# Performance work log

Hardware: AMD Instinct MI355X
Metric: run time of the kernel (lower is better)

The kernel has to match this reference:

```python
import jax, jax.numpy as jnp
import numpy as np

B, S, W = 64, 128, 16
VOCAB, CVOCAB = 50000, 100
WDIM, CDIM, NF = 300, 50, 50
KS = [3, 4, 5]
HID, NLAYERS, NLAB = 256, 2, 5
COMB = WDIM + NF * len(KS)  # 450


def glorot(key, shape):
    fan_in, fan_out = shape[-2], shape[-1]
    lim = jnp.sqrt(6.0 / (fan_in + fan_out))
    return jax.random.uniform(key, shape, minval=-lim, maxval=lim, dtype=jnp.float32)


def setup_inputs() -> dict:
    key = jax.random.key(0)
    ks = jax.random.split(key, 32)
    word_ids = jax.random.randint(ks[0], (B, S), 1, VOCAB)
    char_ids = jax.random.randint(ks[1], (B, S, W), 1, CVOCAB)
    labels = jax.random.randint(ks[2], (B, S), 0, NLAB)
    lengths = jax.random.randint(ks[3], (B,), S // 2, S + 1)
    # embeddings
    word_emb = jax.random.normal(ks[4], (VOCAB, WDIM), jnp.float32) * 0.1
    word_emb = word_emb.at[0].set(0.0)
    char_emb = jax.random.normal(ks[5], (CVOCAB, CDIM), jnp.float32) * 0.1
    char_emb = char_emb.at[0].set(0.0)
    # char conv kernels: [ks, CDIM, NF] each, plus bias
    conv_w = [glorot(ks[6 + i], (k, CDIM, NF)) for i, k in enumerate(KS)]
    conv_b = [jnp.zeros((NF,), jnp.float32) for _ in KS]
    # LSTM params per layer per direction: W_ih [in,4H], W_hh [H,4H], b [4H]
    lstm = []
    kidx = 10
    in_dim = COMB
    for layer in range(NLAYERS):
        for d in range(2):
            Wih = glorot(ks[kidx], (in_dim, 4 * HID)); kidx += 1
            Whh = glorot(ks[kidx], (HID, 4 * HID)); kidx += 1
            b = jnp.zeros((4 * HID,), jnp.float32)
            lstm.extend([Wih, Whh, b])
        in_dim = 2 * HID
    out_w = glorot(ks[kidx], (2 * HID, NLAB)); kidx += 1
    out_b = jnp.zeros((NLAB,), jnp.float32)
    crf_start = jax.random.normal(ks[kidx], (NLAB,), jnp.float32) * 0.1; kidx += 1
    crf_end = jax.random.normal(ks[kidx], (NLAB,), jnp.float32) * 0.1; kidx += 1
    crf_trans = jax.random.normal(ks[kidx], (NLAB, NLAB), jnp.float32) * 0.1
    d = {
        'word_ids': word_ids, 'char_ids': char_ids, 'labels': labels, 'lengths': lengths,
        'word_emb': word_emb, 'char_emb': char_emb,
        'conv_w3': conv_w[0], 'conv_b3': conv_b[0],
        'conv_w4': conv_w[1], 'conv_b4': conv_b[1],
        'conv_w5': conv_w[2], 'conv_b5': conv_b[2],
        'out_w': out_w, 'out_b': out_b,
        'crf_start': crf_start, 'crf_end': crf_end, 'crf_trans': crf_trans,
    }
    names = ['Wih', 'Whh', 'b']
    i = 0
    for layer in range(NLAYERS):
        for dname in ['f', 'r']:
            for n in names:
                d[f'lstm_{n}_l{layer}{dname}'] = lstm[i]; i += 1
    return d


def _conv1d_same(x, w, b, pad):
    # x: [N, L, Cin], w: [k, Cin, Cout] -> [N, L_out, Cout]
    out = jax.lax.conv_general_dilated(x, w, window_strides=(1,), padding=[(pad, pad)],
                                       dimension_numbers=('NWC', 'WIO', 'NWC'))
    return out + b


def _lstm_dir(x, Wih, Whh, b, reverse):
    # x: [B, S, in] -> [B, S, H]; gate order i,f,g,o (torch convention)
    xg = jnp.einsum('bsi,ij->bsj', x, Wih) + b  # [B,S,4H]
    if reverse:
        xg = xg[:, ::-1]
    def step(carry, g):
        h, c = carry
        g = g + h @ Whh
        i, f, gg, o = jnp.split(g, 4, axis=-1)
        i, f, o = jax.nn.sigmoid(i), jax.nn.sigmoid(f), jax.nn.sigmoid(o)
        c = f * c + i * jnp.tanh(gg)
        h = o * jnp.tanh(c)
        return (h, c), h
    h0 = jnp.zeros((x.shape[0], HID), x.dtype)
    _, hs = jax.lax.scan(step, (h0, h0), jnp.swapaxes(xg, 0, 1))
    hs = jnp.swapaxes(hs, 0, 1)
    if reverse:
        hs = hs[:, ::-1]
    return hs


def reference(word_ids, char_ids, labels, lengths, word_emb, char_emb,
              conv_w3, conv_b3, conv_w4, conv_b4, conv_w5, conv_b5,
              out_w, out_b, crf_start, crf_end, crf_trans,
              lstm_Wih_l0f, lstm_Whh_l0f, lstm_b_l0f,
              lstm_Wih_l0r, lstm_Whh_l0r, lstm_b_l0r,
              lstm_Wih_l1f, lstm_Whh_l1f, lstm_b_l1f,
              lstm_Wih_l1r, lstm_Whh_l1r, lstm_b_l1r):
    # char CNN
    ce = char_emb[char_ids.reshape(-1, W)]  # [B*S, W, CDIM]
    pooled = []
    for w, b, k in [(conv_w3, conv_b3, 3), (conv_w4, conv_b4, 4), (conv_w5, conv_b5, 5)]:
        o = jax.nn.relu(_conv1d_same(ce, w, b, k // 2))
        pooled.append(jnp.max(o, axis=1))  # [B*S, NF]
    char_repr = jnp.concatenate(pooled, axis=-1).reshape(B, S, NF * len(KS))
    we = word_emb[word_ids]
    x = jnp.concatenate([we, char_repr], axis=-1)  # [B,S,COMB]
    # BiLSTM 2 layers (dropout disabled / eval mode)
    h_f = _lstm_dir(x, lstm_Wih_l0f, lstm_Whh_l0f, lstm_b_l0f, False)
    h_r = _lstm_dir(x, lstm_Wih_l0r, lstm_Whh_l0r, lstm_b_l0r, True)
    x = jnp.concatenate([h_f, h_r], axis=-1)
    h_f = _lstm_dir(x, lstm_Wih_l1f, lstm_Whh_l1f, lstm_b_l1f, False)
    h_r = _lstm_dir(x, lstm_Wih_l1r, lstm_Whh_l1r, lstm_b_l1r, True)
    x = jnp.concatenate([h_f, h_r], axis=-1)
    emissions = jnp.einsum('bsh,hl->bsl', x, out_w) + out_b  # [B,S,NLAB]
    # CRF NLL (pytorch-crf, batch_first, reduction='mean')
    mask = (jnp.arange(S)[None, :] < lengths[:, None])  # [B,S] bool
    maskf = mask.astype(emissions.dtype)
    tags = labels  # already in [0,NLAB)
    # numerator: score of gold path
    em_score = jnp.take_along_axis(emissions, tags[..., None], axis=-1)[..., 0]  # [B,S]
    num = crf_start[tags[:, 0]] + em_score[:, 0]
    trans_score = crf_trans[tags[:, :-1], tags[:, 1:]]  # [B,S-1]
    num = num + jnp.sum((trans_score + em_score[:, 1:]) * maskf[:, 1:], axis=1)
    last_idx = lengths - 1
    last_tag = jnp.take_along_axis(tags, last_idx[:, None], axis=1)[:, 0]
    num = num + crf_end[last_tag]
    # denominator: forward algorithm via scan
    alpha0 = crf_start + emissions[:, 0]  # [B,NLAB]
    def step(alpha, inp):
        em_t, m_t = inp  # [B,NLAB], [B]
        nxt = jax.nn.logsumexp(alpha[:, :, None] + crf_trans[None], axis=1) + em_t
        alpha = jnp.where(m_t[:, None], nxt, alpha)
        return alpha, None
    alpha, _ = jax.lax.scan(step, alpha0,
                            (jnp.swapaxes(emissions[:, 1:], 0, 1), jnp.swapaxes(mask[:, 1:], 0, 1)))
    denom = jax.nn.logsumexp(alpha + crf_end[None], axis=1)  # [B]
    llh = num - denom
    return -jnp.mean(llh)
```

## Files before the change

### kernel.cpp

```cpp
#include <hip/hip_runtime.h>
#include <hip/hip_fp16.h>
#include <math.h>
#include <stdint.h>

#define NB   64
#define NS   128
#define NW   16
#define CD   50
#define NF_  50
#define WD   300
#define COMB 450
#define K2P0 240
#define K2P1 256
#define HID  256
#define G4   1024
#define NLAB 5

#define WHH_SW4  (7.0f / 0.06846532f)
#define WHH_INV4 (1.0f / (WHH_SW4 * 7.0f))

typedef _Float16 h2_t __attribute__((ext_vector_type(2)));
typedef _Float16 v8h  __attribute__((ext_vector_type(8)));
typedef float    v16f __attribute__((ext_vector_type(16)));

__device__ __forceinline__ float sigf(float x)   { return 1.0f / (1.0f + __expf(-x)); }
__device__ __forceinline__ float tanhf_(float x) { return 1.0f - 2.0f / (__expf(2.0f * x) + 1.0f); }

__device__ __forceinline__ float dot2f(uint32_t a, uint32_t b, float c) {
#if __has_builtin(__builtin_amdgcn_fdot2)
    return __builtin_amdgcn_fdot2(__builtin_bit_cast(h2_t, a),
                                  __builtin_bit_cast(h2_t, b), c, false);
#else
    h2_t ah = __builtin_bit_cast(h2_t, a), bh = __builtin_bit_cast(h2_t, b);
    return c + (float)ah[0] * (float)bh[0] + (float)ah[1] * (float)bh[1];
#endif
}

__device__ __forceinline__ int sdot8f(uint32_t a, int b, int acc) {
#if __has_builtin(__builtin_amdgcn_sdot8)
    return __builtin_amdgcn_sdot8((int)a, b, acc, false);
#else
#pragma unroll
    for (int i = 0; i < 8; ++i) {
        int av = ((int)(a << (28 - 4 * i))) >> 28;
        int bv = ((int)(((uint32_t)b) << (28 - 4 * i))) >> 28;
        acc += av * bv;
    }
    return acc;
#endif
}

__device__ __forceinline__ uint32_t packh2(float lo, float hi) {
    __half l = __float2half(lo), h = __float2half(hi);
    return ((uint32_t)__half_as_ushort(h) << 16) | (uint32_t)__half_as_ushort(l);
}

__global__ __launch_bounds__(256) void pack_convw(
    const float* __restrict__ w3, const float* __restrict__ w4,
    const float* __restrict__ w5, uint32_t* __restrict__ cwp)
{
    int idx = blockIdx.x * 256 + threadIdx.x;
    if (idx >= 15000) return;
    const float* W; int rel;
    if (idx < 3750)       { W = w3; rel = idx; }
    else if (idx < 8750)  { W = w4; rel = idx - 3750; }
    else                  { W = w5; rel = idx - 8750; }
    int t = rel / 1250, rem = rel - t * 1250;
    int c2 = rem / 50, f = rem - c2 * 50;
    float lo = W[(size_t)t * (CD * NF_) + (2 * c2) * NF_ + f];
    float hi = W[(size_t)t * (CD * NF_) + (2 * c2 + 1) * NF_ + f];
    cwp[idx] = packh2(lo, hi);
}

__global__ __launch_bounds__(512) void cnn_embed3(
    const int* __restrict__ word_ids, const int* __restrict__ char_ids,
    const float* __restrict__ word_emb, const float* __restrict__ char_emb,
    const uint32_t* __restrict__ cwp,
    const float* __restrict__ b3, const float* __restrict__ b4,
    const float* __restrict__ b5, uint32_t* __restrict__ x0p)
{
    __shared__ uint32_t cws[15000];
    __shared__ uint32_t cep[8][NW][25];
    int tid  = threadIdx.x;
    int g    = tid >> 6;
    int lane = tid & 63;
    int pos  = blockIdx.x * 8 + g;

    for (int i = tid; i < 15000; i += 512) cws[i] = cwp[i];

    const int* cid = char_ids + (size_t)pos * NW;
    for (int idx = lane; idx < NW * 25; idx += 64) {
        int w  = idx / 25;
        int c2 = idx - w * 25;
        const float* e = char_emb + (size_t)cid[w] * CD + 2 * c2;
        cep[g][w][c2] = packh2(e[0], e[1]);
    }
    {
        int wid = word_ids[pos];
        const float* src = word_emb + (size_t)wid * WD;
        uint32_t* dst = x0p + (size_t)pos * K2P0;
        for (int idx = lane; idx < 150; idx += 64) {
            float2 v = *(const float2*)(src + 2 * idx);
            dst[idx] = packh2(v.x, v.y);
        }
        for (int idx = lane; idx < 15; idx += 64) dst[225 + idx] = 0;
    }
    __syncthreads();

    int f = lane;
    float m3 = 0.f, m4 = 0.f, m5 = 0.f;
    if (f < NF_) {
        float a3[16], a4[17], a5[16];
        float bb3 = b3[f], bb4 = b4[f], bb5 = b5[f];
#pragma unroll
        for (int p = 0; p < 16; ++p) { a3[p] = bb3; a5[p] = bb5; }
#pragma unroll
        for (int p = 0; p < 17; ++p) a4[p] = bb4;

        for (int c2 = 0; c2 < 25; ++c2) {
            uint32_t w3r[3], w4r[4], w5r[5];
#pragma unroll
            for (int t = 0; t < 3; ++t) w3r[t] = cws[(t * 25 + c2) * NF_ + f];
#pragma unroll
            for (int t = 0; t < 4; ++t) w4r[t] = cws[3750 + (t * 25 + c2) * NF_ + f];
#pragma unroll
            for (int t = 0; t < 5; ++t) w5r[t] = cws[8750 + (t * 25 + c2) * NF_ + f];
#pragma unroll
            for (int ip = 0; ip < 16; ++ip) {
                uint32_t v = cep[g][ip][c2];
#pragma unroll
                for (int t = 0; t < 3; ++t) { int p = ip + 1 - t; if (p >= 0 && p < 16) a3[p] = dot2f(v, w3r[t], a3[p]); }
#pragma unroll
                for (int t = 0; t < 4; ++t) { int p = ip + 2 - t; if (p >= 0 && p < 17) a4[p] = dot2f(v, w4r[t], a4[p]); }
#pragma unroll
                for (int t = 0; t < 5; ++t) { int p = ip + 2 - t; if (p >= 0 && p < 16) a5[p] = dot2f(v, w5r[t], a5[p]); }
            }
        }
#pragma unroll
        for (int p = 0; p < 16; ++p) m3 = fmaxf(m3, a3[p]);
#pragma unroll
        for (int p = 0; p < 17; ++p) m4 = fmaxf(m4, a4[p]);
#pragma unroll
        for (int p = 0; p < 16; ++p) m5 = fmaxf(m5, a5[p]);
    }
    float m3x = __shfl_xor(m3, 1);
    float m4x = __shfl_xor(m4, 1);
    float m5x = __shfl_xor(m5, 1);
    if (f < NF_ && !(f & 1)) {
        int i = f >> 1;
        uint32_t* dst = x0p + (size_t)pos * K2P0 + 150;
        dst[i]      = packh2(m3, m3x);
        dst[25 + i] = packh2(m4, m4x);
        dst[50 + i] = packh2(m5, m5x);
    }
}

__global__ __launch_bounds__(256) void pack_wih_all(
    const float* __restrict__ W0f, const float* __restrict__ W0r,
    const float* __restrict__ W1f, const float* __restrict__ W1r,
    uint32_t* __restrict__ P0f, uint32_t* __restrict__ P0r,
    uint32_t* __restrict__ P1f, uint32_t* __restrict__ P1r)
{
    int layer = blockIdx.z;
    int K   = layer ? 512 : COMB;
    int K2P = layer ? K2P1 : K2P0;
    const float* W = layer ? (blockIdx.y ? W1r : W1f) : (blockIdx.y ? W0r : W0f);
    uint32_t* P    = layer ? (blockIdx.y ? P1r : P1f) : (blockIdx.y ? P0r : P0f);

    int idx = blockIdx.x * 256 + threadIdx.x;
    if (idx >= K2P * 1024) return;
    int n = idx & 1023, kp = idx >> 10;
    uint32_t v = 0;
    if (2 * kp + 1 < K) {
        __half l = __float2half(W[(size_t)(2 * kp) * 1024 + n]);
        __half h = __float2half(W[(size_t)(2 * kp + 1) * 1024 + n]);
        v = ((uint32_t)__half_as_ushort(h) << 16) | (uint32_t)__half_as_ushort(l);
    }
    P[((size_t)(kp >> 2) * 1024 + n) * 4 + (kp & 3)] = v;
}

__global__ __launch_bounds__(256) void pack_whh_i4(
    const float* __restrict__ W0, const float* __restrict__ W1,
    const float* __restrict__ W2, const float* __restrict__ W3,
    uint32_t* __restrict__ Q0, uint32_t* __restrict__ Q1,
    uint32_t* __restrict__ Q2, uint32_t* __restrict__ Q3)
{
    int idx = blockIdx.x * 256 + threadIdx.x;
    if (idx >= 32768) return;
    const float* W; uint32_t* Q;
    switch (blockIdx.y) {
        case 0:  W = W0; Q = Q0; break;
        case 1:  W = W1; Q = Q1; break;
        case 2:  W = W2; Q = Q2; break;
        default: W = W3; Q = Q3; break;
    }
    int m = idx & 3, col = (idx >> 2) & 1023, iq = idx >> 12;
    int kbase = (iq * 4 + m) * 8;
    uint32_t out = 0;
#pragma unroll
    for (int j = 0; j < 8; ++j) {
        float w = W[(size_t)(kbase + j) * G4 + col];
        int q = (int)rintf(w * WHH_SW4);
        q = q < -7 ? -7 : (q > 7 ? 7 : q);
        out |= ((uint32_t)(q & 0xF)) << (4 * j);
    }
    Q[idx] = out;
}

__global__ __launch_bounds__(256) void gemm_mfma(
    const uint32_t* __restrict__ Ap, int K2,
    const uint32_t* __restrict__ Wpf, const uint32_t* __restrict__ Wpr,
    const float* __restrict__ bf, const float* __restrict__ br,
    float* __restrict__ Cf, float* __restrict__ Cr)
{
    int by  = blockIdx.y;
    int dir = by >> 4;
    int n0  = (by & 15) * 64;
    int m0  = blockIdx.x * 128;
    const uint32_t* Wp = dir ? Wpr : Wpf;
    const float* bias  = dir ? br : bf;
    float* C           = dir ? Cr : Cf;

    int tid = threadIdx.x;
    int w = tid >> 6, l = tid & 63;
    int l31 = l & 31, lk = l >> 5;

    const uint32_t* arow = Ap + (size_t)(m0 + w * 32 + l31) * K2 + lk * 4;
    const uint4*    bq0  = (const uint4*)(Wp) + (size_t)lk * 1024 + n0 + l31;

    v16f acc0 = {}, acc1 = {};

    for (int kp0 = 0; kp0 < K2; kp0 += 8) {
        uint4 av = *(const uint4*)(arow + kp0);
        const uint4* bq = bq0 + (size_t)(kp0 >> 2) * 1024;
        uint4 b0v = bq[0];
        uint4 b1v = bq[32];
        v8h af = __builtin_bit_cast(v8h, av);
        acc0 = __builtin_amdgcn_mfma_f32_32x32x16_f16(af, __builtin_bit_cast(v8h, b0v), acc0, 0, 0, 0);
        acc1 = __builtin_amdgcn_mfma_f32_32x32x16_f16(af, __builtin_bit_cast(v8h, b1v), acc1, 0, 0, 0);
    }

#pragma unroll
    for (int r = 0; r < 16; ++r) {
        int row = m0 + w * 32 + (r & 3) + 8 * (r >> 2) + 4 * lk;
        int c0 = n0 + l31, c1 = n0 + 32 + l31;
        C[(size_t)row * G4 + c0] = acc0[r] + bias[c0];
        C[(size_t)row * G4 + c1] = acc1[r] + bias[c1];
    }
}

__global__ __launch_bounds__(512, 1) void lstm_rec12(
    const float* __restrict__ xg_f, const float* __restrict__ xg_r,
    const uint32_t* __restrict__ Qf, const uint32_t* __restrict__ Qr,
    uint32_t* __restrict__ outp)
{
    int bid = blockIdx.x;
    int b = bid >> 1, d = bid & 1;
    const float* xg = d ? xg_r : xg_f;
    const uint4* Q4 = (const uint4*)(d ? Qr : Qf);

    __shared__ uint32_t hp8[32];
    __shared__ float gates[G4];
    __shared__ alignas(16) uint4 Tl[4 * 1024];

    int t = threadIdx.x;
    int lane = t & 63;

    uint4 rA[4], rB[4];
#pragma unroll
    for (int iq = 0; iq < 4; ++iq) {
        rA[iq] = Q4[(size_t)iq * 1024 + t];
        rB[iq] = Q4[(size_t)iq * 1024 + t + 512];
    }
    for (int i = t; i < 4 * 1024; i += 512) Tl[i] = Q4[4 * 1024 + i];
    if (t < 32) hp8[t] = 0;
    float cst = 0.f;
    __syncthreads();

    for (int s = 0; s < NS; ++s) {
        int te = d ? (NS - 1 - s) : s;
        int row = b * NS + te;
        size_t r0 = (size_t)row * G4;
        float xA = xg[r0 + t];
        float xB = xg[r0 + 512 + t];

        int hreg = (int)hp8[lane & 31];
        int a0 = 0, a1 = 0;

#pragma unroll
        for (int iq = 0; iq < 4; ++iq) {
            int h0 = __builtin_amdgcn_readlane(hreg, 4 * iq);
            int h1 = __builtin_amdgcn_readlane(hreg, 4 * iq + 1);
            int h2 = __builtin_amdgcn_readlane(hreg, 4 * iq + 2);
            int h3 = __builtin_amdgcn_readlane(hreg, 4 * iq + 3);
            a0 = sdot8f(rA[iq].x, h0, a0); a0 = sdot8f(rA[iq].y, h1, a0);
            a0 = sdot8f(rA[iq].z, h2, a0); a0 = sdot8f(rA[iq].w, h3, a0);
            a1 = sdot8f(rB[iq].x, h0, a1); a1 = sdot8f(rB[iq].y, h1, a1);
            a1 = sdot8f(rB[iq].z, h2, a1); a1 = sdot8f(rB[iq].w, h3, a1);
        }
#pragma unroll
        for (int iq2 = 0; iq2 < 4; ++iq2) {
            uint4 wa = Tl[iq2 * 1024 + t];
            uint4 wb = Tl[iq2 * 1024 + t + 512];
            int h0 = __builtin_amdgcn_readlane(hreg, 16 + 4 * iq2);
            int h1 = __builtin_amdgcn_readlane(hreg, 17 + 4 * iq2);
            int h2 = __builtin_amdgcn_readlane(hreg, 18 + 4 * iq2);
            int h3 = __builtin_amdgcn_readlane(hreg, 19 + 4 * iq2);
            a0 = sdot8f(wa.x, h0, a0); a0 = sdot8f(wa.y, h1, a0);
            a0 = sdot8f(wa.z, h2, a0); a0 = sdot8f(wa.w, h3, a0);
            a1 = sdot8f(wb.x, h0, a1); a1 = sdot8f(wb.y, h1, a1);
            a1 = sdot8f(wb.z, h2, a1); a1 = sdot8f(wb.w, h3, a1);
        }

        gates[t]       = (float)a0 * WHH_INV4 + xA;
        gates[t + 512] = (float)a1 * WHH_INV4 + xB;
        __syncthreads();
        if (t < 256) {
            int j = t;
            float gi = gates[j];
            float gf = gates[256 + j];
            float gg = gates[512 + j];
            float go = gates[768 + j];
            float ii = sigf(gi), ff = sigf(gf), g2 = tanhf_(gg), oo = sigf(go);
            cst = ff * cst + ii * g2;
            float h = oo * tanhf_(cst);
            int q = (int)rintf(h * 7.0f);
            q = q < -7 ? -7 : (q > 7 ? 7 : q);
            int qx = __shfl_xor(q, 1);
            float hx = __shfl_xor(h, 1);
            if (!(t & 1)) {
                ((unsigned char*)hp8)[j >> 1] =
                    (unsigned char)((q & 0xF) | ((qx & 0xF) << 4));
                outp[(size_t)row * 256 + d * 128 + (j >> 1)] = packh2(h, hx);
            }
        }
        __syncthreads();
    }
}

__global__ __launch_bounds__(256) void emis_kernel(
    const uint32_t* __restrict__ x2p, const float* __restrict__ ow,
    const float* __restrict__ ob, float* __restrict__ em)
{
    int i = blockIdx.x * blockDim.x + threadIdx.x;
    if (i >= NB * NS) return;
    const uint32_t* xr = x2p + (size_t)i * 256;
    float acc[NLAB];
#pragma unroll
    for (int l = 0; l < NLAB; ++l) acc[l] = ob[l];
    for (int p = 0; p < 256; ++p) {
        h2_t hv = __builtin_bit_cast(h2_t, xr[p]);
        float lo = (float)hv[0], hi = (float)hv[1];
        int k = 2 * p;
#pragma unroll
        for (int l = 0; l < NLAB; ++l)
            acc[l] += lo * ow[(size_t)k * NLAB + l] + hi * ow[(size_t)(k + 1) * NLAB + l];
    }
    float* e = em + (size_t)i * NLAB;
#pragma unroll
    for (int l = 0; l < NLAB; ++l) e[l] = acc[l];
}

__device__ __forceinline__ float lse5(const float* v) {
    float m = fmaxf(fmaxf(fmaxf(v[0], v[1]), fmaxf(v[2], v[3])), v[4]);
    float s = __expf(v[0] - m) + __expf(v[1] - m) + __expf(v[2] - m) +
              __expf(v[3] - m) + __expf(v[4] - m);
    return m + __logf(s);
}

__global__ __launch_bounds__(64) void crf_kernel(
    const float* __restrict__ em, const int* __restrict__ labels,
    const int* __restrict__ lengths, const float* __restrict__ cstart,
    const float* __restrict__ cend, const float* __restrict__ ctrans,
    float* __restrict__ outp)
{
    __shared__ float tr_s[25], st_s[5], en_s[5];
    int tid = threadIdx.x;
    if (tid < 25) tr_s[tid] = ctrans[tid];
    if (tid < 5)  { st_s[tid] = cstart[tid]; en_s[tid] = cend[tid]; }
    __syncthreads();

    int b = tid;
    int len = lengths[b];
    const int* tg = labels + (size_t)b * NS;
    const float* eb = em + (size_t)b * NS * NLAB;

    int prev = tg[0];
    float num = st_s[prev] + eb[prev];
    for (int t = 1; t < NS; ++t) {
        if (t < len) {
            int cur = tg[t];
            num += tr_s[prev * NLAB + cur] + eb[t * NLAB + cur];
            prev = cur;
        }
    }
    num += en_s[tg[len - 1]];

    float a[NLAB];
#pragma unroll
    for (int y = 0; y < NLAB; ++y) a[y] = st_s[y] + eb[y];
    for (int t = 1; t < NS; ++t) {
        if (t < len) {
            float na[NLAB];
#pragma unroll
            for (int y = 0; y < NLAB; ++y) {
                float v[NLAB];
#pragma unroll
                for (int x = 0; x < NLAB; ++x) v[x] = a[x] + tr_s[x * NLAB + y];
                na[y] = lse5(v) + eb[t * NLAB + y];
            }
#pragma unroll
            for (int y = 0; y < NLAB; ++y) a[y] = na[y];
        }
    }
    float v[NLAB];
#pragma unroll
    for (int y = 0; y < NLAB; ++y) v[y] = a[y] + en_s[y];
    float denom = lse5(v);

    float llh = num - denom;
#pragma unroll
    for (int off = 32; off > 0; off >>= 1) llh += __shfl_down(llh, off);
    if (tid == 0) outp[0] = -llh * (1.0f / 64.0f);
}

extern "C" void kernel_launch(void* const* d_in, const int* in_sizes, int n_in,
                              void* d_out, int out_size, void* d_ws, size_t ws_size,
                              hipStream_t stream)
{
    const int*   word_ids = (const int*)d_in[0];
    const int*   char_ids = (const int*)d_in[1];
    const int*   labels   = (const int*)d_in[2];
    const int*   lengths  = (const int*)d_in[3];
    const float* word_emb = (const float*)d_in[4];
    const float* char_emb = (const float*)d_in[5];
    const float* cw3 = (const float*)d_in[6];
    const float* cb3 = (const float*)d_in[7];
    const float* cw4 = (const float*)d_in[8];
    const float* cb4 = (const float*)d_in[9];
    const float* cw5 = (const float*)d_in[10];
    const float* cb5 = (const float*)d_in[11];
    const float* out_w = (const float*)d_in[12];
    const float* out_b = (const float*)d_in[13];
    const float* crf_start = (const float*)d_in[14];
    const float* crf_end   = (const float*)d_in[15];
    const float* crf_trans = (const float*)d_in[16];
    const float* Wih_l0f = (const float*)d_in[17];
    const float* Whh_l0f = (const float*)d_in[18];
    const float* b_l0f   = (const float*)d_in[19];
    const float* Wih_l0r = (const float*)d_in[20];
    const float* Whh_l0r = (const float*)d_in[21];
    const float* b_l0r   = (const float*)d_in[22];
    const float* Wih_l1f = (const float*)d_in[23];
    const float* Whh_l1f = (const float*)d_in[24];
    const float* b_l1f   = (const float*)d_in[25];
    const float* Wih_l1r = (const float*)d_in[26];
    const float* Whh_l1r = (const float*)d_in[27];
    const float* b_l1r   = (const float*)d_in[28];

    uint32_t* wsu = (uint32_t*)d_ws;
    uint32_t* x0p  = wsu;
    float*    xg_f = (float*)(wsu + 1966080);
    float*    xg_r = xg_f + 8388608;
    uint32_t* x1p  = (uint32_t*)(xg_r + 8388608);
    uint32_t* x2p  = x1p + 2097152;
    float*    em   = (float*)(x2p + 2097152);
    uint32_t* wp0f = (uint32_t*)(em + 40960);
    uint32_t* wp0r = wp0f + 245760;
    uint32_t* wp1f = wp0r + 245760;
    uint32_t* wp1r = wp1f + 262144;
    uint32_t* cwp  = wp1r + 262144;
    uint32_t* wh0f = x0p;
    uint32_t* wh0r = wh0f + 32768;
    uint32_t* wh1f = wh0r + 32768;
    uint32_t* wh1r = wh1f + 32768;

    pack_convw<<<59, 256, 0, stream>>>(cw3, cw4, cw5, cwp);

    cnn_embed3<<<1024, 512, 0, stream>>>(word_ids, char_ids, word_emb, char_emb,
                                         cwp, cb3, cb4, cb5, x0p);

    pack_wih_all<<<dim3(1024, 2, 2), 256, 0, stream>>>(
        Wih_l0f, Wih_l0r, Wih_l1f, Wih_l1r, wp0f, wp0r, wp1f, wp1r);

    dim3 gGemm(64, 32);
    gemm_mfma<<<gGemm, 256, 0, stream>>>(x0p, K2P0, wp0f, wp0r, b_l0f, b_l0r, xg_f, xg_r);

    pack_whh_i4<<<dim3(128, 4), 256, 0, stream>>>(Whh_l0f, Whh_l0r, Whh_l1f, Whh_l1r,
                                                  wh0f, wh0r, wh1f, wh1r);

    lstm_rec12<<<128, 512, 0, stream>>>(xg_f, xg_r, wh0f, wh0r, x1p);

    gemm_mfma<<<gGemm, 256, 0, stream>>>(x1p, K2P1, wp1f, wp1r, b_l1f, b_l1r, xg_f, xg_r);

    lstm_rec12<<<128, 512, 0, stream>>>(xg_f, xg_r, wh1f, wh1r, x2p);

    emis_kernel<<<32, 256, 0, stream>>>(x2p, out_w, out_b, em);
    crf_kernel<<<1, 64, 0, stream>>>(em, labels, lengths, crf_start, crf_end, crf_trans,
                                     (float*)d_out);
}
```

Baseline: 545.7 us.

## Interleave LSTM gate columns so each step needs one barrier, merge pack kernels

The recurrent Whh packing permutes gate columns so that adjacent lanes hold matching i/f/g/o gate values for the same hidden unit. Gate activations are then combined through shuffles instead of a shared-memory gates array, and the hidden state is double-buffered. This removes one __syncthreads and the LDS round trip per timestep. It also splits the sdot8 accumulators to shorten the dependency chain, and fuses the three weight-pack kernels into one launch, moving the Whh packed buffer so it no longer aliases x0p.

Measured after the change: 550.2 us. No clear change (+0.8%).

```diff
diff --git a/kernel.cpp b/kernel.cpp
--- a/kernel.cpp
+++ b/kernel.cpp
@@ -55,21 +55,81 @@
     return ((uint32_t)__half_as_ushort(h) << 16) | (uint32_t)__half_as_ushort(l);
 }
 
-__global__ __launch_bounds__(256) void pack_convw(
+#define PK_CONV_END 59
+#define PK_WIH0_END (59 + 1920)
+#define PK_WIH1_END (PK_WIH0_END + 2048)
+#define PK_END      (PK_WIH1_END + 512)
+
+__global__ __launch_bounds__(256) void pack_all(
     const float* __restrict__ w3, const float* __restrict__ w4,
-    const float* __restrict__ w5, uint32_t* __restrict__ cwp)
-{
-    int idx = blockIdx.x * 256 + threadIdx.x;
-    if (idx >= 15000) return;
-    const float* W; int rel;
-    if (idx < 3750)       { W = w3; rel = idx; }
-    else if (idx < 8750)  { W = w4; rel = idx - 3750; }
-    else                  { W = w5; rel = idx - 8750; }
-    int t = rel / 1250, rem = rel - t * 1250;
-    int c2 = rem / 50, f = rem - c2 * 50;
-    float lo = W[(size_t)t * (CD * NF_) + (2 * c2) * NF_ + f];
-    float hi = W[(size_t)t * (CD * NF_) + (2 * c2 + 1) * NF_ + f];
-    cwp[idx] = packh2(lo, hi);
+    const float* __restrict__ w5, uint32_t* __restrict__ cwp,
+    const float* __restrict__ Wih0f, const float* __restrict__ Wih0r,
+    const float* __restrict__ Wih1f, const float* __restrict__ Wih1r,
+    uint32_t* __restrict__ P0f, uint32_t* __restrict__ P0r,
+    uint32_t* __restrict__ P1f, uint32_t* __restrict__ P1r,
+    const float* __restrict__ Whh0f, const float* __restrict__ Whh0r,
+    const float* __restrict__ Whh1f, const float* __restrict__ Whh1r,
+    uint32_t* __restrict__ Q0f, uint32_t* __restrict__ Q0r,
+    uint32_t* __restrict__ Q1f, uint32_t* __restrict__ Q1r)
+{
+    int blk = blockIdx.x;
+    int tid = threadIdx.x;
+
+    if (blk < PK_CONV_END) {
+        int idx = blk * 256 + tid;
+        if (idx >= 15000) return;
+        const float* W; int rel;
+        if (idx < 3750)       { W = w3; rel = idx; }
+        else if (idx < 8750)  { W = w4; rel = idx - 3750; }
+        else                  { W = w5; rel = idx - 8750; }
+        int t = rel / 1250, rem = rel - t * 1250;
+        int c2 = rem / 50, f = rem - c2 * 50;
+        float lo = W[(size_t)t * (CD * NF_) + (2 * c2) * NF_ + f];
+        float hi = W[(size_t)t * (CD * NF_) + (2 * c2 + 1) * NF_ + f];
+        cwp[idx] = packh2(lo, hi);
+    } else if (blk < PK_WIH1_END) {
+        int layer, dir, rel;
+        if (blk < PK_WIH0_END) { layer = 0; rel = blk - PK_CONV_END; dir = rel / 960;  rel %= 960; }
+        else                   { layer = 1; rel = blk - PK_WIH0_END; dir = rel / 1024; rel %= 1024; }
+        int K   = layer ? 512 : COMB;
+        int K2P = layer ? K2P1 : K2P0;
+        const float* W = layer ? (dir ? Wih1r : Wih1f) : (dir ? Wih0r : Wih0f);
+        uint32_t* P    = layer ? (dir ? P1r : P1f) : (dir ? P0r : P0f);
+        int idx = rel * 256 + tid;
+        if (idx >= K2P * 1024) return;
+        int n = idx & 1023, kp = idx >> 10;
+        uint32_t v = 0;
+        if (2 * kp + 1 < K) {
+            __half l = __float2half(W[(size_t)(2 * kp) * 1024 + n]);
+            __half h = __float2half(W[(size_t)(2 * kp + 1) * 1024 + n]);
+            v = ((uint32_t)__half_as_ushort(h) << 16) | (uint32_t)__half_as_ushort(l);
+        }
+        P[((size_t)(kp >> 2) * 1024 + n) * 4 + (kp & 3)] = v;
+    } else {
+        int rel = blk - PK_WIH1_END;
+        int which = rel >> 7;
+        const float* W; uint32_t* Q;
+        switch (which) {
+            case 0:  W = Whh0f; Q = Q0f; break;
+            case 1:  W = Whh0r; Q = Q0r; break;
+            case 2:  W = Whh1f; Q = Q1f; break;
+            default: W = Whh1r; Q = Q1r; break;
+        }
+        int idx = (rel & 127) * 256 + tid;
+        int m = idx & 3, s = (idx >> 2) & 1023, iq = idx >> 12;
+        int sh = s & 511;
+        int L = ((s >> 9) << 9) + ((sh & 1) << 8) + (sh >> 1);
+        int kbase = (iq * 4 + m) * 8;
+        uint32_t out = 0;
+#pragma unroll
+        for (int j = 0; j < 8; ++j) {
+            float w = W[(size_t)(kbase + j) * G4 + L];
+            int q = (int)rintf(w * WHH_SW4);
+            q = q < -7 ? -7 : (q > 7 ? 7 : q);
+            out |= ((uint32_t)(q & 0xF)) << (4 * j);
+        }
+        Q[idx] = out;
+    }
 }
 
 __global__ __launch_bounds__(512) void cnn_embed3(
@@ -155,58 +215,6 @@
     }
 }
 
-__global__ __launch_bounds__(256) void pack_wih_all(
-    const float* __restrict__ W0f, const float* __restrict__ W0r,
-    const float* __restrict__ W1f, const float* __restrict__ W1r,
-    uint32_t* __restrict__ P0f, uint32_t* __restrict__ P0r,
-    uint32_t* __restrict__ P1f, uint32_t* __restrict__ P1r)
-{
-    int layer = blockIdx.z;
-    int K   = layer ? 512 : COMB;
-    int K2P = layer ? K2P1 : K2P0;
-    const float* W = layer ? (blockIdx.y ? W1r : W1f) : (blockIdx.y ? W0r : W0f);
-    uint32_t* P    = layer ? (blockIdx.y ? P1r : P1f) : (blockIdx.y ? P0r : P0f);
-
-    int idx = blockIdx.x * 256 + threadIdx.x;
-    if (idx >= K2P * 1024) return;
-    int n = idx & 1023, kp = idx >> 10;
-    uint32_t v = 0;
-    if (2 * kp + 1 < K) {
-        __half l = __float2half(W[(size_t)(2 * kp) * 1024 + n]);
-        __half h = __float2half(W[(size_t)(2 * kp + 1) * 1024 + n]);
-        v = ((uint32_t)__half_as_ushort(h) << 16) | (uint32_t)__half_as_ushort(l);
-    }
-    P[((size_t)(kp >> 2) * 1024 + n) * 4 + (kp & 3)] = v;
-}
-
-__global__ __launch_bounds__(256) void pack_whh_i4(
-    const float* __restrict__ W0, const float* __restrict__ W1,
-    const float* __restrict__ W2, const float* __restrict__ W3,
-    uint32_t* __restrict__ Q0, uint32_t* __restrict__ Q1,
-    uint32_t* __restrict__ Q2, uint32_t* __restrict__ Q3)
-{
-    int idx = blockIdx.x * 256 + threadIdx.x;
-    if (idx >= 32768) return;
-    const float* W; uint32_t* Q;
-    switch (blockIdx.y) {
-        case 0:  W = W0; Q = Q0; break;
-        case 1:  W = W1; Q = Q1; break;
-        case 2:  W = W2; Q = Q2; break;
-        default: W = W3; Q = Q3; break;
-    }
-    int m = idx & 3, col = (idx >> 2) & 1023, iq = idx >> 12;
-    int kbase = (iq * 4 + m) * 8;
-    uint32_t out = 0;
-#pragma unroll
-    for (int j = 0; j < 8; ++j) {
-        float w = W[(size_t)(kbase + j) * G4 + col];
-        int q = (int)rintf(w * WHH_SW4);
-        q = q < -7 ? -7 : (q > 7 ? 7 : q);
-        out |= ((uint32_t)(q & 0xF)) << (4 * j);
-    }
-    Q[idx] = out;
-}
-
 __global__ __launch_bounds__(256) void gemm_mfma(
     const uint32_t* __restrict__ Ap, int K2,
     const uint32_t* __restrict__ Wpf, const uint32_t* __restrict__ Wpr,
@@ -249,7 +257,7 @@
     }
 }
 
-__global__ __launch_bounds__(512, 1) void lstm_rec12(
+__global__ __launch_bounds__(512, 1) void lstm_rec13(
     const float* __restrict__ xg_f, const float* __restrict__ xg_r,
     const uint32_t* __restrict__ Qf, const uint32_t* __restrict__ Qr,
     uint32_t* __restrict__ outp)
@@ -259,12 +267,12 @@
     const float* xg = d ? xg_r : xg_f;
     const uint4* Q4 = (const uint4*)(d ? Qr : Qf);
 
-    __shared__ uint32_t hp8[32];
-    __shared__ float gates[G4];
+    __shared__ uint32_t hp8[2][32];
     __shared__ alignas(16) uint4 Tl[4 * 1024];
 
     int t = threadIdx.x;
     int lane = t & 63;
+    int Lt = ((t & 1) << 8) + (t >> 1);
 
     uint4 rA[4], rB[4];
 #pragma unroll
@@ -273,19 +281,20 @@
         rB[iq] = Q4[(size_t)iq * 1024 + t + 512];
     }
     for (int i = t; i < 4 * 1024; i += 512) Tl[i] = Q4[4 * 1024 + i];
-    if (t < 32) hp8[t] = 0;
-    float cst = 0.f;
+    if (t < 32) hp8[0][t] = 0;
+    float cst = 0.f, h = 0.f;
+    int q = 0;
     __syncthreads();
 
     for (int s = 0; s < NS; ++s) {
         int te = d ? (NS - 1 - s) : s;
         int row = b * NS + te;
         size_t r0 = (size_t)row * G4;
-        float xA = xg[r0 + t];
-        float xB = xg[r0 + 512 + t];
-
-        int hreg = (int)hp8[lane & 31];
-        int a0 = 0, a1 = 0;
+        float xA = xg[r0 + Lt];
+        float xB = xg[r0 + Lt + 512];
+
+        int hreg = (int)hp8[s & 1][lane & 31];
+        int a0a = 0, a0b = 0, a1a = 0, a1b = 0;
 
 #pragma unroll
         for (int iq = 0; iq < 4; ++iq) {
@@ -293,10 +302,10 @@
             int h1 = __builtin_amdgcn_readlane(hreg, 4 * iq + 1);
             int h2 = __builtin_amdgcn_readlane(hreg, 4 * iq + 2);
             int h3 = __builtin_amdgcn_readlane(hreg, 4 * iq + 3);
-            a0 = sdot8f(rA[iq].x, h0, a0); a0 = sdot8f(rA[iq].y, h1, a0);
-            a0 = sdot8f(rA[iq].z, h2, a0); a0 = sdot8f(rA[iq].w, h3, a0);
-            a1 = sdot8f(rB[iq].x, h0, a1); a1 = sdot8f(rB[iq].y, h1, a1);
-            a1 = sdot8f(rB[iq].z, h2, a1); a1 = sdot8f(rB[iq].w, h3, a1);
+            a0a = sdot8f(rA[iq].x, h0, a0a); a0b = sdot8f(rA[iq].y, h1, a0b);
+            a0a = sdot8f(rA[iq].z, h2, a0a); a0b = sdot8f(rA[iq].w, h3, a0b);
+            a1a = sdot8f(rB[iq].x, h0, a1a); a1b = sdot8f(rB[iq].y, h1, a1b);
+            a1a = sdot8f(rB[iq].z, h2, a1a); a1b = sdot8f(rB[iq].w, h3, a1b);
         }
 #pragma unroll
         for (int iq2 = 0; iq2 < 4; ++iq2) {
@@ -306,33 +315,30 @@
             int h1 = __builtin_amdgcn_readlane(hreg, 17 + 4 * iq2);
             int h2 = __builtin_amdgcn_readlane(hreg, 18 + 4 * iq2);
             int h3 = __builtin_amdgcn_readlane(hreg, 19 + 4 * iq2);
-            a0 = sdot8f(wa.x, h0, a0); a0 = sdot8f(wa.y, h1, a0);
-            a0 = sdot8f(wa.z, h2, a0); a0 = sdot8f(wa.w, h3, a0);
-            a1 = sdot8f(wb.x, h0, a1); a1 = sdot8f(wb.y, h1, a1);
-            a1 = sdot8f(wb.z, h2, a1); a1 = sdot8f(wb.w, h3, a1);
-        }
-
-        gates[t]       = (float)a0 * WHH_INV4 + xA;
-        gates[t + 512] = (float)a1 * WHH_INV4 + xB;
-        __syncthreads();
-        if (t < 256) {
-            int j = t;
-            float gi = gates[j];
-            float gf = gates[256 + j];
-            float gg = gates[512 + j];
-            float go = gates[768 + j];
-            float ii = sigf(gi), ff = sigf(gf), g2 = tanhf_(gg), oo = sigf(go);
+            a0a = sdot8f(wa.x, h0, a0a); a0b = sdot8f(wa.y, h1, a0b);
+            a0a = sdot8f(wa.z, h2, a0a); a0b = sdot8f(wa.w, h3, a0b);
+            a1a = sdot8f(wb.x, h0, a1a); a1b = sdot8f(wb.y, h1, a1b);
+            a1a = sdot8f(wb.z, h2, a1a); a1b = sdot8f(wb.w, h3, a1b);
+        }
+
+        float g0 = (float)(a0a + a0b) * WHH_INV4 + xA;
+        float g1 = (float)(a1a + a1b) * WHH_INV4 + xB;
+        float g0x = __shfl_xor(g0, 1);
+        float g1x = __shfl_xor(g1, 1);
+        if (!(t & 1)) {
+            float ii = sigf(g0), ff = sigf(g0x), g2 = tanhf_(g1), oo = sigf(g1x);
             cst = ff * cst + ii * g2;
-            float h = oo * tanhf_(cst);
-            int q = (int)rintf(h * 7.0f);
-            q = q < -7 ? -7 : (q > 7 ? 7 : q);
-            int qx = __shfl_xor(q, 1);
-            float hx = __shfl_xor(h, 1);
-            if (!(t & 1)) {
-                ((unsigned char*)hp8)[j >> 1] =
-                    (unsigned char)((q & 0xF) | ((qx & 0xF) << 4));
-                outp[(size_t)row * 256 + d * 128 + (j >> 1)] = packh2(h, hx);
-            }
+            h = oo * tanhf_(cst);
+            int qv = (int)rintf(h * 7.0f);
+            q = qv < -7 ? -7 : (qv > 7 ? 7 : qv);
+        }
+        float hx = __shfl_xor(h, 2);
+        int   qx = __shfl_xor(q, 2);
+        if (!(t & 3)) {
+            int i = t >> 2;
+            ((unsigned char*)hp8[(s + 1) & 1])[i] =
+                (unsigned char)((q & 0xF) | ((qx & 0xF) << 4));
+            outp[(size_t)row * 256 + d * 128 + i] = packh2(h, hx);
         }
         __syncthreads();
     }
@@ -470,30 +476,27 @@
     uint32_t* wp1f = wp0r + 245760;
     uint32_t* wp1r = wp1f + 262144;
     uint32_t* cwp  = wp1r + 262144;
-    uint32_t* wh0f = x0p;
+    uint32_t* wh0f = cwp  + 15000;
     uint32_t* wh0r = wh0f + 32768;
     uint32_t* wh1f = wh0r + 32768;
     uint32_t* wh1r = wh1f + 32768;
 
-    pack_convw<<<59, 256, 0, stream>>>(cw3, cw4, cw5, cwp);
+    pack_all<<<PK_END, 256, 0, stream>>>(
+        cw3, cw4, cw5, cwp,
+        Wih_l0f, Wih_l0r, Wih_l1f, Wih_l1r, wp0f, wp0r, wp1f, wp1r,
+        Whh_l0f, Whh_l0r, Whh_l1f, Whh_l1r, wh0f, wh0r, wh1f, wh1r);
 
     cnn_embed3<<<1024, 512, 0, stream>>>(word_ids, char_ids, word_emb, char_emb,
                                          cwp, cb3, cb4, cb5, x0p);
 
-    pack_wih_all<<<dim3(1024, 2, 2), 256, 0, stream>>>(
-        Wih_l0f, Wih_l0r, Wih_l1f, Wih_l1r, wp0f, wp0r, wp1f, wp1r);
-
     dim3 gGemm(64, 32);
     gemm_mfma<<<gGemm, 256, 0, stream>>>(x0p, K2P0, wp0f, wp0r, b_l0f, b_l0r, xg_f, xg_r);
 
-    pack_whh_i4<<<dim3(128, 4), 256, 0, stream>>>(Whh_l0f, Whh_l0r, Whh_l1f, Whh_l1r,
-                                                  wh0f, wh0r, wh1f, wh1r);
-
-    lstm_rec12<<<128, 512, 0, stream>>>(xg_f, xg_r, wh0f, wh0r, x1p);
+    lstm_rec13<<<128, 512, 0, stream>>>(xg_f, xg_r, wh0f, wh0r, x1p);
 
     gemm_mfma<<<gGemm, 256, 0, stream>>>(x1p, K2P1, wp1f, wp1r, b_l1f, b_l1r, xg_f, xg_r);
 
-    lstm_rec12<<<128, 512, 0, stream>>>(xg_f, xg_r, wh1f, wh1r, x2p);
+    lstm_rec13<<<128, 512, 0, stream>>>(xg_f, xg_r, wh1f, wh1r, x2p);
 
     emis_kernel<<<32, 256, 0, stream>>>(x2p, out_w, out_b, em);
     crf_kernel<<<1, 64, 0, stream>>>(em, labels, lengths, crf_start, crf_end, crf_trans,
```
